# Kernel tuning notes

Hardware: AMD Instinct MI355X
Metric: run time of the kernel (lower is better)

Reference implementation:

```python
import jax, jax.numpy as jnp
from jax import lax
import numpy as np

B, T, V, E, U = 1024, 80, 50000, 512, 512


def setup_inputs() -> dict:
    key = jax.random.key(0)
    ks = jax.random.split(key, 6)
    return {
        "tokens": jax.random.randint(ks[0], (B, T), 0, V, dtype=jnp.int32),
        "emb": jax.random.normal(ks[1], (V, E), jnp.float32) * 0.05,
        "kernel": jax.random.normal(ks[2], (E, U), jnp.float32) * (1.0 / np.sqrt(E)),
        "rec_kernel": jax.random.normal(ks[3], (U, U), jnp.float32) * (1.0 / np.sqrt(U)),
        "bias": jnp.zeros((U,), jnp.float32),
        "fc_w": jax.random.normal(ks[4], (U, 1), jnp.float32) * (1.0 / np.sqrt(U)),
        "fc_b": jnp.zeros((1,), jnp.float32),
    }


def reference(tokens, emb, kernel, rec_kernel, bias, fc_w, fc_b):
    # Embedding lookup: [B, T] -> [B, T, E]
    x = emb[tokens]
    # Precompute input projection for all timesteps (one big GEMM): [B, T, U]
    xk = jnp.einsum("bte,eu->btu", x, kernel) + bias
    h0 = jnp.zeros((tokens.shape[0], rec_kernel.shape[0]), dtype=emb.dtype)

    def step(h, xt):  # SimpleRNNCell (eval mode): h' = tanh(x@W + h@R + b)
        h_new = jnp.tanh(xt + h @ rec_kernel)
        return h_new, None

    h_final, _ = lax.scan(step, h0, jnp.swapaxes(xk, 0, 1))  # scan over T
    logits = h_final @ fc_w + fc_b  # [B, 1]
    return jax.nn.sigmoid(logits)
```

## Files before the change

kernel.cpp:

```cpp
#include <hip/hip_runtime.h>
#include <stdint.h>

constexpr int NB = 1024;
constexpr int NT = 80;
constexpr int NV = 50000;
constexpr int NE = 512;
constexpr int NU = 512;

typedef __attribute__((ext_vector_type(8))) __bf16 bf16x8;
typedef __attribute__((ext_vector_type(4))) float f32x4;
typedef __attribute__((ext_vector_type(4))) uint16_t u16x4;
typedef __attribute__((ext_vector_type(4))) float float4v;
typedef __attribute__((ext_vector_type(4))) uint32_t u32x4;

__device__ __forceinline__ uint16_t f2bf(float f) {
  uint32_t u = __builtin_bit_cast(uint32_t, f);
  u += 0x7FFFu + ((u >> 16) & 1u);
  return (uint16_t)(u >> 16);
}
__device__ __forceinline__ float bf2f(uint16_t h) {
  uint32_t u = ((uint32_t)h) << 16;
  return __builtin_bit_cast(float, u);
}
__device__ __forceinline__ float tanh_fast(float x) {
  float e = __expf(2.0f * x);
  return 1.0f - 2.0f / (e + 1.0f);
}

__device__ __forceinline__ void store16_cc(uint16_t* p, u32x4 v) {
  asm volatile("global_store_dwordx4 %0, %1, off sc0 sc1" :: "v"(p), "v"(v) : "memory");
}
__device__ __forceinline__ u32x4 load16_cc(const uint16_t* p) {
  u32x4 r;
  asm volatile("global_load_dwordx4 %0, %1, off sc0 sc1" : "=v"(r) : "v"(p) : "memory");
  return r;
}


__global__ __launch_bounds__(256) void emb_to_bf16(const float* __restrict__ in,
                                                   uint16_t* __restrict__ out) {
  int i = blockIdx.x * 256 + threadIdx.x;
  float4v v = ((const float4v*)in)[i];
  u16x4 o;
  o.x = f2bf(v.x); o.y = f2bf(v.y); o.z = f2bf(v.z); o.w = f2bf(v.w);
  ((u16x4*)out)[i] = o;
}

__global__ __launch_bounds__(256) void pack_w(const float* __restrict__ w,
                                              uint16_t* __restrict__ out) {
  int idx = blockIdx.x * 256 + threadIdx.x;
  int lane = idx & 63;
  int ks = (idx >> 6) & 15;
  int nt = idx >> 10;
  int n  = nt * 16 + (lane & 15);
  int k0 = ks * 32 + (lane >> 4) * 8;
  uint16_t v[8];
#pragma unroll
  for (int j = 0; j < 8; j++) v[j] = f2bf(w[(size_t)(k0 + j) * NU + n]);
  u16x4* o = (u16x4*)(out + (size_t)idx * 8);
  o[0] = (u16x4){v[0], v[1], v[2], v[3]};
  o[1] = (u16x4){v[4], v[5], v[6], v[7]};
}

__global__ __launch_bounds__(256, 2) void proj_gemm(const int* __restrict__ tokens,
                                                    const uint16_t* __restrict__ embb,
                                                    const uint16_t* __restrict__ kpack,
                                                    const float* __restrict__ bias,
                                                    uint16_t* __restrict__ xkp) {
  int wave = threadIdx.x >> 6;
  int lane = threadIdx.x & 63;
  int ln15 = lane & 15;
  int quad = lane >> 4;
  int m0 = blockIdx.x * 64;
  int t = m0 >> 10;
  int b0 = m0 & 1023;

  int tok[4];
#pragma unroll
  for (int mt = 0; mt < 4; mt++)
    tok[mt] = tokens[(size_t)(b0 + mt * 16 + ln15) * NT + t];

  float bv[8];
#pragma unroll
  for (int nt = 0; nt < 8; nt++) bv[nt] = bias[wave * 128 + nt * 16 + ln15];

  f32x4 acc[4][8];
#pragma unroll
  for (int mt = 0; mt < 4; mt++)
#pragma unroll
    for (int nt = 0; nt < 8; nt++) acc[mt][nt] = (f32x4){0.f, 0.f, 0.f, 0.f};

  bf16x8 aC[4], aN[4];
#pragma unroll
  for (int mt = 0; mt < 4; mt++) {
    aC[mt] = *(const bf16x8*)(embb + (size_t)tok[mt] * NE + 0 * 32 + quad * 8);
    aN[mt] = *(const bf16x8*)(embb + (size_t)tok[mt] * NE + 1 * 32 + quad * 8);
  }

#pragma unroll 1
  for (int ks = 0; ks < 16; ks++) {
    bf16x8 aF[4];
    int ksn = (ks + 2) & 15;
#pragma unroll
    for (int mt = 0; mt < 4; mt++)
      aF[mt] = *(const bf16x8*)(embb + (size_t)tok[mt] * NE + ksn * 32 + quad * 8);
#pragma unroll
    for (int nt = 0; nt < 8; nt++) {
      int ntg = wave * 8 + nt;
      bf16x8 bfr = *(const bf16x8*)(kpack + (((size_t)ntg * 16 + ks) * 64 + lane) * 8);
#pragma unroll
      for (int mt = 0; mt < 4; mt++)
        acc[mt][nt] = __builtin_amdgcn_mfma_f32_16x16x32_bf16(aC[mt], bfr, acc[mt][nt], 0, 0, 0);
    }
#pragma unroll
    for (int mt = 0; mt < 4; mt++) { aC[mt] = aN[mt]; aN[mt] = aF[mt]; }
  }

#pragma unroll
  for (int mt = 0; mt < 4; mt++) {
    int g = (b0 >> 4) + mt;
#pragma unroll
    for (int nt = 0; nt < 8; nt++) {
      int ntg = wave * 8 + nt;
      size_t tile = ((size_t)t * 64 + g) * 32 + ntg;
      u16x4 o;
      o.x = f2bf(acc[mt][nt][0] + bv[nt]);
      o.y = f2bf(acc[mt][nt][1] + bv[nt]);
      o.z = f2bf(acc[mt][nt][2] + bv[nt]);
      o.w = f2bf(acc[mt][nt][3] + bv[nt]);
      *(u16x4*)(xkp + tile * 256 + (size_t)lane * 4) = o;
    }
  }
}

__global__ __launch_bounds__(256, 1)
void rnn_rec(const uint16_t* __restrict__ xkp,
             const uint16_t* __restrict__ rpack,
             const float* __restrict__ fcw,
             const float* __restrict__ fcb,
             uint16_t* __restrict__ hx,
             int* __restrict__ flags,
             float* __restrict__ out) {
  __shared__ uint16_t hS[16 * 16 * 4 * 8];

  const int bid = blockIdx.x;
  const int g = bid & 63, s = bid >> 6;
  const int wave = threadIdx.x >> 6, lane = threadIdx.x & 63;
  const int ln15 = lane & 15, quad = lane >> 4;
  const int ntg0 = s * 8 + wave * 2;

  bf16x8 bf0[16], bf1[16];
#pragma unroll
  for (int ks = 0; ks < 16; ks++) {
    bf0[ks] = *(const bf16x8*)(rpack + (((size_t)(ntg0 + 0) * 16 + ks) * 64 + lane) * 8);
    bf1[ks] = *(const bf16x8*)(rpack + (((size_t)(ntg0 + 1) * 16 + ks) * 64 + lane) * 8);
  }

  {
    u32x4 z = (u32x4){0u, 0u, 0u, 0u};
#pragma unroll
    for (int i = 0; i < 4; i++) ((u32x4*)hS)[i * 256 + threadIdx.x] = z;
  }
  __syncthreads();

  int* myflag = flags + (g * 4 + s) * 16;

  for (int t = 0; t < NT; t++) {
    const uint16_t* xb = xkp + (((size_t)t * 64 + g) * 32) * 256;
    u16x4 xv0 = *(const u16x4*)(xb + (size_t)(ntg0 + 0) * 256 + (size_t)lane * 4);
    u16x4 xv1 = *(const u16x4*)(xb + (size_t)(ntg0 + 1) * 256 + (size_t)lane * 4);

    f32x4 acc0 = (f32x4){0.f, 0.f, 0.f, 0.f};
    f32x4 acc1 = (f32x4){0.f, 0.f, 0.f, 0.f};
#pragma unroll
    for (int ks = 0; ks < 16; ks++) {
      bf16x8 a = *(const bf16x8*)(hS + (size_t)ks * 512 + ln15 * 32 + quad * 8);
      acc0 = __builtin_amdgcn_mfma_f32_16x16x32_bf16(a, bf0[ks], acc0, 0, 0, 0);
      acc1 = __builtin_amdgcn_mfma_f32_16x16x32_bf16(a, bf1[ks], acc1, 0, 0, 0);
    }

    uint16_t hv0[4], hv1[4];
#pragma unroll
    for (int r = 0; r < 4; r++) {
      hv0[r] = f2bf(tanh_fast(acc0[r] + bf2f(xv0[r])));
      hv1[r] = f2bf(tanh_fast(acc1[r] + bf2f(xv1[r])));
    }

    __syncthreads();

#pragma unroll
    for (int i = 0; i < 2; i++) {
      int col128 = (wave * 2 + i) * 16 + ln15;
      int kloc = col128 >> 5, qw = (col128 >> 3) & 3, j = col128 & 7;
      const uint16_t* hv = (i == 0) ? hv0 : hv1;
#pragma unroll
      for (int r = 0; r < 4; r++) {
        int row = quad * 4 + r;
        hS[(size_t)(s * 4 + kloc) * 512 + row * 32 + qw * 8 + j] = hv[r];
      }
    }
    __syncthreads();

    {
      u32x4 d = *(const u32x4*)(hS + (size_t)s * 2048 + (size_t)threadIdx.x * 8);
      uint16_t* dst = hx + ((size_t)((t + 1) & 1) * 256 + g * 4 + s) * 2048 +
                      (size_t)threadIdx.x * 8;
      store16_cc(dst, d);
      asm volatile("s_waitcnt vmcnt(0)" ::: "memory");
    }
    __syncthreads();

    if (threadIdx.x == 0)
      __hip_atomic_store(myflag, t + 1, __ATOMIC_RELAXED, __HIP_MEMORY_SCOPE_AGENT);

    if (wave > 0) {
      int sp = (s + wave) & 3;
      int* fp = flags + (g * 4 + sp) * 16;
      int spin = 0;
      while (__hip_atomic_load(fp, __ATOMIC_RELAXED, __HIP_MEMORY_SCOPE_AGENT) < t + 1 &&
             spin < (1 << 16))
        spin++;
      asm volatile("" ::: "memory");
      const uint16_t* src = hx + ((size_t)((t + 1) & 1) * 256 + g * 4 + sp) * 2048;
      u32x4 v[4];
#pragma unroll
      for (int i = 0; i < 4; i++) v[i] = load16_cc(src + (size_t)(i * 64 + lane) * 8);
      asm volatile("s_waitcnt vmcnt(0)" ::: "memory");
#pragma unroll
      for (int i = 0; i < 4; i++)
        *(u32x4*)(hS + (size_t)sp * 2048 + (size_t)(i * 64 + lane) * 8) = v[i];
    }
    __syncthreads();
  }

  if (s == 0) {
#pragma unroll
    for (int rr = 0; rr < 4; rr++) {
      int row = wave * 4 + rr;
      const uint16_t* hr = hS + (size_t)(lane >> 2) * 512 + row * 32 + (lane & 3) * 8;
      float p = 0.f;
#pragma unroll
      for (int j = 0; j < 8; j++) p += bf2f(hr[j]) * fcw[lane * 8 + j];
#pragma unroll
      for (int off = 32; off; off >>= 1) p += __shfl_down(p, off);
      if (lane == 0) {
        float logit = p + fcb[0];
        out[g * 16 + row] = 1.0f / (1.0f + __expf(-logit));
      }
    }
  }
}

extern "C" void kernel_launch(void* const* d_in, const int* in_sizes, int n_in,
                              void* d_out, int out_size, void* d_ws, size_t ws_size,
                              hipStream_t stream) {
  const int* tokens   = (const int*)d_in[0];
  const float* emb    = (const float*)d_in[1];
  const float* kernel_w = (const float*)d_in[2];
  const float* rec_w  = (const float*)d_in[3];
  const float* bias   = (const float*)d_in[4];
  const float* fcw    = (const float*)d_in[5];
  const float* fcb    = (const float*)d_in[6];
  float* out = (float*)d_out;

  uint16_t* embb  = (uint16_t*)d_ws;
  uint16_t* kpack = embb + (size_t)NV * NE;
  uint16_t* rpack = kpack + (size_t)NE * NU;
  uint16_t* xkp   = rpack + (size_t)NU * NU;
  uint16_t* hx    = xkp + (size_t)NT * NB * NU;
  int* flags      = (int*)(hx + (size_t)2 * 256 * 2048);

  hipLaunchKernelGGL(emb_to_bf16, dim3(25000), dim3(256), 0, stream, emb, embb);
  hipLaunchKernelGGL(pack_w, dim3(128), dim3(256), 0, stream, kernel_w, kpack);
  hipLaunchKernelGGL(pack_w, dim3(128), dim3(256), 0, stream, rec_w, rpack);
  hipLaunchKernelGGL(proj_gemm, dim3(1280), dim3(256), 0, stream, tokens, embb, kpack, bias, xkp);
  hipLaunchKernelGGL(rnn_rec, dim3(256), dim3(256), 0, stream, xkp, rpack, fcw, fcb, hx, flags, out);
}
```

Measured before the change: 454.4 us.

## Double-buffer recurrent state and use per-wave flags to cut block barriers

The recurrent kernel's shared hidden-state buffer is double-buffered, so each wave writes its own slice and publishes it to global memory with its own per-wave flag. The four block-wide barriers per timestep shrink to one. Consumer waves poll the four per-wave flags of each peer block. The input-projection load is prefetched one step ahead, and the MFMA chain is split into two independent accumulators to shorten the dependency chain. This adds more flag traffic and a subtler ordering scheme in exchange for fewer synchronisations on the serial critical path.

```diff
diff --git a/kernel.cpp b/kernel.cpp
--- a/kernel.cpp
+++ b/kernel.cpp
@@ -141,43 +141,53 @@
              uint16_t* __restrict__ hx,
              int* __restrict__ flags,
              float* __restrict__ out) {
-  __shared__ uint16_t hS[16 * 16 * 4 * 8];
+  __shared__ uint16_t hS[2][16 * 512];
 
   const int bid = blockIdx.x;
   const int g = bid & 63, s = bid >> 6;
   const int wave = threadIdx.x >> 6, lane = threadIdx.x & 63;
   const int ln15 = lane & 15, quad = lane >> 4;
   const int ntg0 = s * 8 + wave * 2;
+  const int region = s * 4 + wave;
 
   bf16x8 bf0[16], bf1[16];
 #pragma unroll
   for (int ks = 0; ks < 16; ks++) {
     bf0[ks] = *(const bf16x8*)(rpack + (((size_t)(ntg0 + 0) * 16 + ks) * 64 + lane) * 8);
     bf1[ks] = *(const bf16x8*)(rpack + (((size_t)(ntg0 + 1) * 16 + ks) * 64 + lane) * 8);
+    asm volatile("" : "+v"(bf0[ks]));
+    asm volatile("" : "+v"(bf1[ks]));
   }
 
   {
     u32x4 z = (u32x4){0u, 0u, 0u, 0u};
 #pragma unroll
-    for (int i = 0; i < 4; i++) ((u32x4*)hS)[i * 256 + threadIdx.x] = z;
+    for (int i = 0; i < 4; i++) ((u32x4*)hS[0])[i * 256 + threadIdx.x] = z;
   }
   __syncthreads();
 
-  int* myflag = flags + (g * 4 + s) * 16;
+  u16x4 xv0 = *(const u16x4*)(xkp + ((size_t)(0 * 64 + g) * 32 + ntg0 + 0) * 256 + (size_t)lane * 4);
+  u16x4 xv1 = *(const u16x4*)(xkp + ((size_t)(0 * 64 + g) * 32 + ntg0 + 1) * 256 + (size_t)lane * 4);
 
   for (int t = 0; t < NT; t++) {
-    const uint16_t* xb = xkp + (((size_t)t * 64 + g) * 32) * 256;
-    u16x4 xv0 = *(const u16x4*)(xb + (size_t)(ntg0 + 0) * 256 + (size_t)lane * 4);
-    u16x4 xv1 = *(const u16x4*)(xb + (size_t)(ntg0 + 1) * 256 + (size_t)lane * 4);
-
-    f32x4 acc0 = (f32x4){0.f, 0.f, 0.f, 0.f};
-    f32x4 acc1 = (f32x4){0.f, 0.f, 0.f, 0.f};
-#pragma unroll
-    for (int ks = 0; ks < 16; ks++) {
-      bf16x8 a = *(const bf16x8*)(hS + (size_t)ks * 512 + ln15 * 32 + quad * 8);
-      acc0 = __builtin_amdgcn_mfma_f32_16x16x32_bf16(a, bf0[ks], acc0, 0, 0, 0);
-      acc1 = __builtin_amdgcn_mfma_f32_16x16x32_bf16(a, bf1[ks], acc1, 0, 0, 0);
-    }
+    const uint16_t* hc = hS[t & 1];
+    uint16_t* hn = hS[(t + 1) & 1];
+    const int par = (t + 1) & 1;
+
+    f32x4 a0a = (f32x4){0.f, 0.f, 0.f, 0.f}, a0b = a0a, a1a = a0a, a1b = a0a;
+#pragma unroll
+    for (int ks = 0; ks < 8; ks++) {
+      bf16x8 a = *(const bf16x8*)(hc + (size_t)ks * 512 + ln15 * 32 + quad * 8);
+      a0a = __builtin_amdgcn_mfma_f32_16x16x32_bf16(a, bf0[ks], a0a, 0, 0, 0);
+      a1a = __builtin_amdgcn_mfma_f32_16x16x32_bf16(a, bf1[ks], a1a, 0, 0, 0);
+    }
+#pragma unroll
+    for (int ks = 8; ks < 16; ks++) {
+      bf16x8 a = *(const bf16x8*)(hc + (size_t)ks * 512 + ln15 * 32 + quad * 8);
+      a0b = __builtin_amdgcn_mfma_f32_16x16x32_bf16(a, bf0[ks], a0b, 0, 0, 0);
+      a1b = __builtin_amdgcn_mfma_f32_16x16x32_bf16(a, bf1[ks], a1b, 0, 0, 0);
+    }
+    f32x4 acc0 = a0a + a0b, acc1 = a1a + a1b;
 
     uint16_t hv0[4], hv1[4];
 #pragma unroll
@@ -186,58 +196,62 @@
       hv1[r] = f2bf(tanh_fast(acc1[r] + bf2f(xv1[r])));
     }
 
-    __syncthreads();
-
-#pragma unroll
-    for (int i = 0; i < 2; i++) {
-      int col128 = (wave * 2 + i) * 16 + ln15;
-      int kloc = col128 >> 5, qw = (col128 >> 3) & 3, j = col128 & 7;
-      const uint16_t* hv = (i == 0) ? hv0 : hv1;
+    {
+      int j = ln15 & 7;
+      int qw0 = (ln15 >> 3);
+      int qw1 = 2 + (ln15 >> 3);
+      uint16_t* rg = hn + (size_t)region * 512;
 #pragma unroll
       for (int r = 0; r < 4; r++) {
         int row = quad * 4 + r;
-        hS[(size_t)(s * 4 + kloc) * 512 + row * 32 + qw * 8 + j] = hv[r];
+        rg[row * 32 + qw0 * 8 + j] = hv0[r];
+        rg[row * 32 + qw1 * 8 + j] = hv1[r];
       }
     }
-    __syncthreads();
+    u32x4 d = *(const u32x4*)(hn + (size_t)region * 512 + (size_t)lane * 8);
+    store16_cc(hx + (((size_t)par * 64 + g) * 16 + region) * 512 + (size_t)lane * 8, d);
+    asm volatile("s_waitcnt vmcnt(0)" ::: "memory");
+    if (lane == 0)
+      __hip_atomic_store(flags + g * 16 + region, t + 1, __ATOMIC_RELAXED,
+                         __HIP_MEMORY_SCOPE_AGENT);
 
     {
-      u32x4 d = *(const u32x4*)(hS + (size_t)s * 2048 + (size_t)threadIdx.x * 8);
-      uint16_t* dst = hx + ((size_t)((t + 1) & 1) * 256 + g * 4 + s) * 2048 +
-                      (size_t)threadIdx.x * 8;
-      store16_cc(dst, d);
-      asm volatile("s_waitcnt vmcnt(0)" ::: "memory");
-    }
-    __syncthreads();
-
-    if (threadIdx.x == 0)
-      __hip_atomic_store(myflag, t + 1, __ATOMIC_RELAXED, __HIP_MEMORY_SCOPE_AGENT);
+      int tn = (t + 1 < NT) ? t + 1 : t;
+      xv0 = *(const u16x4*)(xkp + ((size_t)(tn * 64 + g) * 32 + ntg0 + 0) * 256 + (size_t)lane * 4);
+      xv1 = *(const u16x4*)(xkp + ((size_t)(tn * 64 + g) * 32 + ntg0 + 1) * 256 + (size_t)lane * 4);
+    }
 
     if (wave > 0) {
       int sp = (s + wave) & 3;
-      int* fp = flags + (g * 4 + sp) * 16;
+      const int* fp = flags + g * 16 + sp * 4;
       int spin = 0;
-      while (__hip_atomic_load(fp, __ATOMIC_RELAXED, __HIP_MEMORY_SCOPE_AGENT) < t + 1 &&
-             spin < (1 << 16))
+      while (spin < (1 << 16)) {
+        int f0 = __hip_atomic_load(fp + 0, __ATOMIC_RELAXED, __HIP_MEMORY_SCOPE_AGENT);
+        int f1 = __hip_atomic_load(fp + 1, __ATOMIC_RELAXED, __HIP_MEMORY_SCOPE_AGENT);
+        int f2 = __hip_atomic_load(fp + 2, __ATOMIC_RELAXED, __HIP_MEMORY_SCOPE_AGENT);
+        int f3 = __hip_atomic_load(fp + 3, __ATOMIC_RELAXED, __HIP_MEMORY_SCOPE_AGENT);
+        if (f0 >= t + 1 && f1 >= t + 1 && f2 >= t + 1 && f3 >= t + 1) break;
         spin++;
+      }
       asm volatile("" ::: "memory");
-      const uint16_t* src = hx + ((size_t)((t + 1) & 1) * 256 + g * 4 + sp) * 2048;
+      const uint16_t* src = hx + (((size_t)par * 64 + g) * 16 + sp * 4) * 512;
       u32x4 v[4];
 #pragma unroll
-      for (int i = 0; i < 4; i++) v[i] = load16_cc(src + (size_t)(i * 64 + lane) * 8);
+      for (int i = 0; i < 4; i++) v[i] = load16_cc(src + (size_t)(i * 512) + (size_t)lane * 8);
       asm volatile("s_waitcnt vmcnt(0)" ::: "memory");
 #pragma unroll
       for (int i = 0; i < 4; i++)
-        *(u32x4*)(hS + (size_t)sp * 2048 + (size_t)(i * 64 + lane) * 8) = v[i];
-    }
-    __syncthreads();
+        *(u32x4*)(hn + (size_t)(sp * 4 + i) * 512 + (size_t)lane * 8) = v[i];
+    }
+
+    asm volatile("s_waitcnt lgkmcnt(0)\n\ts_barrier" ::: "memory");
   }
 
   if (s == 0) {
 #pragma unroll
     for (int rr = 0; rr < 4; rr++) {
       int row = wave * 4 + rr;
-      const uint16_t* hr = hS + (size_t)(lane >> 2) * 512 + row * 32 + (lane & 3) * 8;
+      const uint16_t* hr = hS[0] + (size_t)(lane >> 2) * 512 + row * 32 + (lane & 3) * 8;
       float p = 0.f;
 #pragma unroll
       for (int j = 0; j < 8; j++) p += bf2f(hr[j]) * fcw[lane * 8 + j];
@@ -268,7 +282,7 @@
   uint16_t* rpack = kpack + (size_t)NE * NU;
   uint16_t* xkp   = rpack + (size_t)NU * NU;
   uint16_t* hx    = xkp + (size_t)NT * NB * NU;
-  int* flags      = (int*)(hx + (size_t)2 * 256 * 2048);
+  int* flags      = (int*)(hx + (size_t)2 * 64 * 16 * 512);
 
   hipLaunchKernelGGL(emb_to_bf16, dim3(25000), dim3(256), 0, stream, emb, embb);
   hipLaunchKernelGGL(pack_w, dim3(128), dim3(256), 0, stream, kernel_w, kpack);
```

Measured after the change: 466.5 us. 2.7% more time.
